# Kernel tuning notes

Measured on AMD Instinct MI355X. Metric: run time of the kernel, lower is better.

Reference implementation:

```python
import jax, jax.numpy as jnp
import numpy as np

M_MARGIN = 0.5
S_SCALE = 30.0
EPS = 1e-12

def _l2norm(a):
    return a / jnp.maximum(jnp.linalg.norm(a, axis=1, keepdims=True), EPS)

def setup_inputs() -> dict:
    key = jax.random.key(0)
    k1, k2, k3 = jax.random.split(key, 3)
    B, D, V = 2048, 512, 32000
    x = jax.random.normal(k1, (B, D), dtype=jnp.float32)
    # kaiming_normal_ on (V, D): std = sqrt(2 / D)
    W = jax.random.normal(k2, (V, D), dtype=jnp.float32) * np.sqrt(2.0 / D)
    labels = jax.random.randint(k3, (B,), 0, V, dtype=jnp.int64)
    return {"x": x, "W": W, "labels": labels}

def reference(x, W, labels):
    cos_m, sin_m = jnp.cos(M_MARGIN), jnp.sin(M_MARGIN)
    nx = _l2norm(x)            # [B, D]
    nW = _l2norm(W)            # [V, D]
    cosine = nx @ nW.T         # [B, V]
    B = cosine.shape[0]
    rows = jnp.arange(B)
    # phi only matters at the label column (phi.where(one_hot, cosine))
    cos_y = cosine[rows, labels]                            # [B]
    sin_y = jnp.sqrt(jnp.clip(1.0 - cos_y * cos_y, 0.0, 1.0))
    phi_y = cos_y * cos_m - sin_y * sin_m                   # [B]
    logits = cosine.at[rows, labels].set(phi_y) * S_SCALE   # [B, V]
    logp = jax.nn.log_softmax(logits, axis=1)
    return -logp[rows, labels].sum() / B
```

## Files before the change

kernel.cpp:

```cpp
#include <hip/hip_runtime.h>
#include <math.h>
#include <stdint.h>

#define B_ROWS 2048
#define D_DIM  512
#define V_COLS 32000
#define BM 128
#define BN 128
#define BK 64
#define KSTEPS (D_DIM / BK)
#define NCT    (V_COLS / BN)
#define S_SC   30.0f
#define COS_M  0.8775825618903728f
#define SIN_M  0.479425538604203f

typedef float f32x4 __attribute__((ext_vector_type(4)));
typedef long  i64x2 __attribute__((ext_vector_type(2)));

__device__ __forceinline__ void load16_to_lds(const void* g, void* l) {
  __builtin_amdgcn_global_load_lds(
      (__attribute__((address_space(1))) void*)(g),
      (__attribute__((address_space(3))) void*)(l),
      16, 0, 0);
}

__global__ void fused_norm_kernel(const float* __restrict__ x,
                                  const float* __restrict__ W,
                                  uint8_t* __restrict__ nx,
                                  uint8_t* __restrict__ nw,
                                  float* __restrict__ rowsum,
                                  float* __restrict__ out) {
  if (blockIdx.x == 0 && threadIdx.x == 0) out[0] = 0.f;
  if (blockIdx.x < B_ROWS / 256) rowsum[blockIdx.x * 256 + threadIdx.x] = 0.f;
  const int lane = threadIdx.x & 63;
  const int wave = threadIdx.x >> 6;
  const int gr   = blockIdx.x * 4 + wave;
  const float* src;
  uint8_t* dst;
  if (gr < B_ROWS) {
    src = x + (size_t)gr * D_DIM;
    dst = nx + (size_t)gr * D_DIM;
  } else {
    src = W + (size_t)(gr - B_ROWS) * D_DIM;
    dst = nw + (size_t)(gr - B_ROWS) * D_DIM;
  }
  const float4* r4 = (const float4*)src;
  float4 v0 = r4[2 * lane];
  float4 v1 = r4[2 * lane + 1];
  float ss = v0.x*v0.x + v0.y*v0.y + v0.z*v0.z + v0.w*v0.w
           + v1.x*v1.x + v1.y*v1.y + v1.z*v1.z + v1.w*v1.w;
  #pragma unroll
  for (int off = 32; off >= 1; off >>= 1) ss += __shfl_xor(ss, off, 64);
  float inv = 1.0f / fmaxf(sqrtf(ss), 1e-12f);
  int p0 = __builtin_amdgcn_cvt_pk_fp8_f32(v0.x * inv, v0.y * inv, 0, false);
  p0     = __builtin_amdgcn_cvt_pk_fp8_f32(v0.z * inv, v0.w * inv, p0, true);
  int p1 = __builtin_amdgcn_cvt_pk_fp8_f32(v1.x * inv, v1.y * inv, 0, false);
  p1     = __builtin_amdgcn_cvt_pk_fp8_f32(v1.z * inv, v1.w * inv, p1, true);
  ((int2*)dst)[lane] = make_int2(p0, p1);
}

__global__ __launch_bounds__(256, 4)
void arc_gemm_kernel(const uint8_t* __restrict__ nx,
                     const uint8_t* __restrict__ nw,
                     const int* __restrict__ labels,
                     float* __restrict__ rowsum,
                     float* __restrict__ lbl_logit) {
  __shared__ uint8_t sA[2][BM * BK];
  __shared__ uint8_t sB[2][BN * BK];

  const int id = blockIdx.x;
  const int ct = ((id >> 7) << 3) | (id & 7);
  if (ct >= NCT) return;
  const int rt = (id >> 3) & 15;
  const int m0 = rt * BM;
  const int n0 = ct * BN;

  const int tid  = threadIdx.x;
  const int wave = tid >> 6;
  const int lane = tid & 63;
  const int wm   = wave >> 1;
  const int wn   = wave & 1;
  const int quad = lane >> 4;
  const int l16  = lane & 15;

  const int srow = tid >> 2;
  const int jg   = (tid & 3) ^ ((srow >> 1) & 3);
  const uint8_t* gA = nx + (size_t)(m0 + srow) * D_DIM + jg * 16;
  const uint8_t* gB = nw + (size_t)(n0 + srow) * D_DIM + jg * 16;
  const int ldsOff0 = wave * 1024;
  const int ldsOff1 = 4096 + wave * 1024;

  const int cSlot = (quad ^ ((l16 >> 1) & 3)) << 4;
  const int aBase = (wm * 64 + l16) * BK + cSlot;
  const int bBase = (wn * 64 + l16) * BK + cSlot;

  f32x4 acc[4][4];
  #pragma unroll
  for (int i = 0; i < 4; ++i)
    #pragma unroll
    for (int j = 0; j < 4; ++j) acc[i][j] = (f32x4){0.f, 0.f, 0.f, 0.f};

  load16_to_lds(gA,              &sA[0][ldsOff0]);
  load16_to_lds(gA + 64 * D_DIM, &sA[0][ldsOff1]);
  load16_to_lds(gB,              &sB[0][ldsOff0]);
  load16_to_lds(gB + 64 * D_DIM, &sB[0][ldsOff1]);

  #pragma unroll
  for (int ks = 0; ks < KSTEPS; ++ks) {
    __syncthreads();
    if (ks + 1 < KSTEPS) {
      const int off = (ks + 1) * BK;
      const int nb  = (ks + 1) & 1;
      load16_to_lds(gA + off,              &sA[nb][ldsOff0]);
      load16_to_lds(gA + 64 * D_DIM + off, &sA[nb][ldsOff1]);
      load16_to_lds(gB + off,              &sB[nb][ldsOff0]);
      load16_to_lds(gB + 64 * D_DIM + off, &sB[nb][ldsOff1]);
    }
    __syncthreads();

    const uint8_t* bA = sA[ks & 1];
    const uint8_t* bB = sB[ks & 1];
    i64x2 a2[4];
    #pragma unroll
    for (int mi = 0; mi < 4; ++mi)
      a2[mi] = *(const i64x2*)(bA + aBase + mi * 16 * BK);
    #pragma unroll
    for (int ni = 0; ni < 4; ++ni) {
      const i64x2 b2 = *(const i64x2*)(bB + bBase + ni * 16 * BK);
      #pragma unroll
      for (int mi = 0; mi < 4; ++mi) {
        acc[mi][ni] = __builtin_amdgcn_mfma_f32_16x16x32_fp8_fp8(a2[mi][0], b2[0], acc[mi][ni], 0, 0, 0);
        acc[mi][ni] = __builtin_amdgcn_mfma_f32_16x16x32_fp8_fp8(a2[mi][1], b2[1], acc[mi][ni], 0, 0, 0);
      }
    }
  }

  const int lblv = labels[m0 + wm * 64 + lane];
  #pragma unroll
  for (int mi = 0; mi < 4; ++mi) {
    #pragma unroll
    for (int r = 0; r < 4; ++r) {
      const int rw   = mi * 16 + quad * 4 + r;
      const int grow = m0 + wm * 64 + rw;
      const int lbl  = __shfl(lblv, rw, 64);
      float rsum = 0.f;
      #pragma unroll
      for (int ni = 0; ni < 4; ++ni) {
        float c = acc[mi][ni][r];
        const int gcol = n0 + wn * 64 + ni * 16 + l16;
        if (gcol == lbl) {
          float sy  = sqrtf(fminf(1.f, fmaxf(0.f, 1.f - c * c)));
          float phi = c * COS_M - sy * SIN_M;
          lbl_logit[grow] = S_SC * phi;
          c = phi;
        }
        rsum += __expf(S_SC * c - 30.0f);
      }
      #pragma unroll
      for (int off = 1; off < 16; off <<= 1)
        rsum += __shfl_xor(rsum, off, 64);
      if (l16 == 0) atomicAdd(&rowsum[grow], rsum);
    }
  }
}

__global__ void arc_finish_kernel(const float* __restrict__ rowsum,
                                  const float* __restrict__ lbl_logit,
                                  float* __restrict__ out) {
  const int row  = blockIdx.x * 256 + threadIdx.x;
  const int lane = threadIdx.x & 63;
  const int wave = threadIdx.x >> 6;
  float v = (30.0f + logf(rowsum[row]) - lbl_logit[row]) * (1.0f / (float)B_ROWS);
  #pragma unroll
  for (int off = 32; off >= 1; off >>= 1) v += __shfl_xor(v, off, 64);
  __shared__ float wsum[4];
  if (lane == 0) wsum[wave] = v;
  __syncthreads();
  if (threadIdx.x == 0) atomicAdd(out, wsum[0] + wsum[1] + wsum[2] + wsum[3]);
}

extern "C" void kernel_launch(void* const* d_in, const int* in_sizes, int n_in,
                              void* d_out, int out_size, void* d_ws, size_t ws_size,
                              hipStream_t stream) {
  const float* x      = (const float*)d_in[0];
  const float* W      = (const float*)d_in[1];
  const int*   labels = (const int*)d_in[2];
  float* out = (float*)d_out;

  char* ws = (char*)d_ws;
  uint8_t* nx = (uint8_t*)ws;
  uint8_t* nw = (uint8_t*)(ws + (size_t)B_ROWS * D_DIM);
  char* p = ws + (size_t)B_ROWS * D_DIM + (size_t)V_COLS * D_DIM;
  float* rowsum    = (float*)p;  p += (size_t)B_ROWS * 4;
  float* lbl_logit = (float*)p;

  hipLaunchKernelGGL(fused_norm_kernel, dim3((B_ROWS + V_COLS) / 4), dim3(256), 0, stream,
                     x, W, nx, nw, rowsum, out);
  hipLaunchKernelGGL(arc_gemm_kernel, dim3(32 * 16 * 8), dim3(256), 0, stream,
                     nx, nw, labels, rowsum, lbl_logit);
  hipLaunchKernelGGL(arc_finish_kernel, dim3(B_ROWS / 256), dim3(256), 0, stream,
                     rowsum, lbl_logit, out);
}
```

Before: 176.1 us.

## Triple-buffer LDS tiles with explicit vmcnt waits in FP8 GEMM loop

Replaces the double-buffered A/B LDS tiles with a three-stage ring buffer and prefetches two K-steps ahead. The __syncthreads pairs become explicit s_waitcnt vmcnt counts plus raw s_barrier, so the global-to-LDS loads for later stages stay in flight while the current tile is computed. This adds 16KB of LDS per block, which may reduce occupancy relative to the launch bound of 4. The hand-written waitcnt values are tied to the exact number of outstanding loads and can break if the compiler reorders memory operations.

```diff
diff --git a/kernel.cpp b/kernel.cpp
--- a/kernel.cpp
+++ b/kernel.cpp
@@ -10,6 +10,7 @@
 #define BK 64
 #define KSTEPS (D_DIM / BK)
 #define NCT    (V_COLS / BN)
+#define TILE_B (BM * BK)
 #define S_SC   30.0f
 #define COS_M  0.8775825618903728f
 #define SIN_M  0.479425538604203f
@@ -65,8 +66,7 @@
                      const int* __restrict__ labels,
                      float* __restrict__ rowsum,
                      float* __restrict__ lbl_logit) {
-  __shared__ uint8_t sA[2][BM * BK];
-  __shared__ uint8_t sB[2][BN * BK];
+  __shared__ uint8_t sMem[3][2 * TILE_B];
 
   const int id = blockIdx.x;
   const int ct = ((id >> 7) << 3) | (id & 7);
@@ -87,12 +87,14 @@
   const int jg   = (tid & 3) ^ ((srow >> 1) & 3);
   const uint8_t* gA = nx + (size_t)(m0 + srow) * D_DIM + jg * 16;
   const uint8_t* gB = nw + (size_t)(n0 + srow) * D_DIM + jg * 16;
-  const int ldsOff0 = wave * 1024;
-  const int ldsOff1 = 4096 + wave * 1024;
+  const int offA0 = wave * 1024;
+  const int offA1 = 4096 + wave * 1024;
+  const int offB0 = TILE_B + wave * 1024;
+  const int offB1 = TILE_B + 4096 + wave * 1024;
 
   const int cSlot = (quad ^ ((l16 >> 1) & 3)) << 4;
   const int aBase = (wm * 64 + l16) * BK + cSlot;
-  const int bBase = (wn * 64 + l16) * BK + cSlot;
+  const int bBase = TILE_B + (wn * 64 + l16) * BK + cSlot;
 
   f32x4 acc[4][4];
   #pragma unroll
@@ -100,39 +102,46 @@
     #pragma unroll
     for (int j = 0; j < 4; ++j) acc[i][j] = (f32x4){0.f, 0.f, 0.f, 0.f};
 
-  load16_to_lds(gA,              &sA[0][ldsOff0]);
-  load16_to_lds(gA + 64 * D_DIM, &sA[0][ldsOff1]);
-  load16_to_lds(gB,              &sB[0][ldsOff0]);
-  load16_to_lds(gB + 64 * D_DIM, &sB[0][ldsOff1]);
+  #pragma unroll
+  for (int t = 0; t < 2; ++t) {
+    load16_to_lds(gA + t * BK,              &sMem[t][offA0]);
+    load16_to_lds(gA + 64 * D_DIM + t * BK, &sMem[t][offA1]);
+    load16_to_lds(gB + t * BK,              &sMem[t][offB0]);
+    load16_to_lds(gB + 64 * D_DIM + t * BK, &sMem[t][offB1]);
+  }
 
   #pragma unroll
   for (int ks = 0; ks < KSTEPS; ++ks) {
-    __syncthreads();
-    if (ks + 1 < KSTEPS) {
-      const int off = (ks + 1) * BK;
-      const int nb  = (ks + 1) & 1;
-      load16_to_lds(gA + off,              &sA[nb][ldsOff0]);
-      load16_to_lds(gA + 64 * D_DIM + off, &sA[nb][ldsOff1]);
-      load16_to_lds(gB + off,              &sB[nb][ldsOff0]);
-      load16_to_lds(gB + 64 * D_DIM + off, &sB[nb][ldsOff1]);
+    if (ks + 2 < KSTEPS) {
+      const int nb  = (ks + 2) % 3;
+      const int off = (ks + 2) * BK;
+      load16_to_lds(gA + off,              &sMem[nb][offA0]);
+      load16_to_lds(gA + 64 * D_DIM + off, &sMem[nb][offA1]);
+      load16_to_lds(gB + off,              &sMem[nb][offB0]);
+      load16_to_lds(gB + 64 * D_DIM + off, &sMem[nb][offB1]);
+      asm volatile("s_waitcnt vmcnt(8)" ::: "memory");
+    } else if (ks + 1 < KSTEPS) {
+      asm volatile("s_waitcnt vmcnt(4)" ::: "memory");
+    } else {
+      asm volatile("s_waitcnt vmcnt(0)" ::: "memory");
     }
-    __syncthreads();
-
-    const uint8_t* bA = sA[ks & 1];
-    const uint8_t* bB = sB[ks & 1];
+    asm volatile("s_barrier" ::: "memory");
+
+    const uint8_t* bA = &sMem[ks % 3][0];
     i64x2 a2[4];
     #pragma unroll
     for (int mi = 0; mi < 4; ++mi)
       a2[mi] = *(const i64x2*)(bA + aBase + mi * 16 * BK);
     #pragma unroll
     for (int ni = 0; ni < 4; ++ni) {
-      const i64x2 b2 = *(const i64x2*)(bB + bBase + ni * 16 * BK);
+      const i64x2 b2 = *(const i64x2*)(bA + bBase + ni * 16 * BK);
       #pragma unroll
       for (int mi = 0; mi < 4; ++mi) {
         acc[mi][ni] = __builtin_amdgcn_mfma_f32_16x16x32_fp8_fp8(a2[mi][0], b2[0], acc[mi][ni], 0, 0, 0);
         acc[mi][ni] = __builtin_amdgcn_mfma_f32_16x16x32_fp8_fp8(a2[mi][1], b2[1], acc[mi][ni], 0, 0, 0);
       }
     }
+    asm volatile("s_waitcnt lgkmcnt(0)\n\ts_barrier" ::: "memory");
   }
 
   const int lblv = labels[m0 + wm * 64 + lane];
```

Measured after the change: 177.3 us. About the same (+0.7%).
